# Performance work log

Hardware: AMD Instinct MI355X
Metric: run time of the kernel (lower is better)

Reference implementation:

```python
import jax, jax.numpy as jnp
import numpy as np

B, S, D = 4, 2048, 1024


def setup_inputs() -> dict:
    key = jax.random.key(0)
    ks = jax.random.split(key, 8)
    x = jax.random.normal(ks[0], (B, S, D), dtype=jnp.float32)
    # additive causal mask: 0 on/below diagonal, -1e9 above
    causal = jnp.tril(jnp.ones((S, S), dtype=bool))
    mask = jnp.where(causal, 0.0, -1e9).astype(jnp.float32)[None, :, :]  # [1,S,S]
    scale = 1.0 / np.sqrt(D)
    Wq = jax.random.normal(ks[1], (D, D), dtype=jnp.float32) * scale
    bq = jnp.zeros((D,), dtype=jnp.float32)
    Wk = jax.random.normal(ks[2], (D, D), dtype=jnp.float32) * scale
    bk = jnp.zeros((D,), dtype=jnp.float32)
    Wv = jax.random.normal(ks[3], (D, D), dtype=jnp.float32) * scale
    bv = jnp.zeros((D,), dtype=jnp.float32)
    return {"x": x, "mask": mask, "Wq": Wq, "bq": bq, "Wk": Wk, "bk": bk, "Wv": Wv, "bv": bv}


def reference(x, mask, Wq, bq, Wk, bk, Wv, bv):
    # Q/K/V projections (torch Linear: y = x @ W^T + b)
    q = jnp.einsum('bsd,ed->bse', x, Wq) + bq
    k = jnp.einsum('bsd,ed->bse', x, Wk) + bk
    v = jnp.einsum('bsd,ed->bse', x, Wv) + bv
    d = x.shape[-1]
    scores = jnp.einsum('bqd,bkd->bqk', q, k) / jnp.sqrt(jnp.float32(d))
    scores = scores + mask
    attn = jax.nn.softmax(scores, axis=-1)
    return jnp.einsum('bqk,bkd->bqd', attn, v)
```

## Files before the change

kernel.cpp:

```cpp
#include <hip/hip_runtime.h>
#include <hip/hip_bf16.h>


typedef __attribute__((ext_vector_type(8))) short short8;
typedef __attribute__((ext_vector_type(4))) float f32x4;
typedef __attribute__((ext_vector_type(4))) unsigned short ushort4v;

static __device__ __forceinline__ unsigned short f2b(float f) {
  union { __hip_bfloat16 h; unsigned short u; } cv;
  cv.h = __float2bfloat16(f);
  return cv.u;
}

#define GLOAD_LDS16(gsrc, ldst)                                              \
  __builtin_amdgcn_global_load_lds(                                          \
      (const __attribute__((address_space(1))) void*)(gsrc),                 \
      (__attribute__((address_space(3))) void*)(ldst), 16, 0, 0)

__global__ __launch_bounds__(256) void cvt4(const float* __restrict__ in,
                                            unsigned short* __restrict__ out, int n4) {
  int i = blockIdx.x * blockDim.x + threadIdx.x;
  if (i >= n4) return;
  float4 v = reinterpret_cast<const float4*>(in)[i];
  ushort4v o;
  o.x = f2b(v.x); o.y = f2b(v.y); o.z = f2b(v.z); o.w = f2b(v.w);
  reinterpret_cast<ushort4v*>(out)[i] = o;
}

__global__ __launch_bounds__(256) void prep_w(
    const float* __restrict__ Wq, const float* __restrict__ Wk, const float* __restrict__ Wv,
    const float* __restrict__ bq, const float* __restrict__ bk, const float* __restrict__ bv,
    unsigned short* __restrict__ Wb, float* __restrict__ biasb) {
  int id = blockIdx.x;
  if (id < 3072) {
    int sel = id >> 10;
    const float* src = sel == 0 ? Wq : sel == 1 ? Wk : Wv;
    int i = (id & 1023) * 256 + threadIdx.x;
    float4 v = reinterpret_cast<const float4*>(src)[i];
    ushort4v o;
    o.x = f2b(v.x); o.y = f2b(v.y); o.z = f2b(v.z); o.w = f2b(v.w);
    reinterpret_cast<ushort4v*>(Wb + (long)sel * 1048576)[i] = o;
  } else {
    int i = (id - 3072) * 256 + threadIdx.x;
    if (i < 3072) {
      int sel = i >> 10;
      const float* src = sel == 0 ? bq : sel == 1 ? bk : bv;
      biasb[i] = src[i & 1023];
    }
  }
}

template <typename EPI>
static __device__ __forceinline__ void gemm128_body(
    const unsigned short* __restrict__ Ab, const unsigned short* __restrict__ Bb,
    int lda, int ldb, int nkt, unsigned short* sA, unsigned short* sB, EPI epi) {
  int tid = threadIdx.x;
  int lane = tid & 63;
  int w = tid >> 6;
  int wr = w >> 1, wc = w & 1;

  f32x4 acc[4][4];
#pragma unroll
  for (int m = 0; m < 4; ++m)
#pragma unroll
    for (int n = 0; n < 4; ++n) acc[m][n] = (f32x4){0.f, 0.f, 0.f, 0.f};

  for (int kt = 0; kt < nkt; ++kt) {
    __syncthreads();
#pragma unroll
    for (int c = 0; c < 8; ++c) {
      int chunk = w * 8 + c;
      int half = chunk & 15;
      int L = half * 1024 + lane * 16;
      int row = L >> 7;
      int gs = ((L >> 4) & 7) ^ (row & 7);
      if (chunk < 16) {
        GLOAD_LDS16(Ab + (long)row * lda + kt * 64 + gs * 8, sA + half * 512);
      } else {
        GLOAD_LDS16(Bb + (long)row * ldb + kt * 64 + gs * 8, sB + half * 512);
      }
    }
    __syncthreads();

#pragma unroll
    for (int kk = 0; kk < 2; ++kk) {
      short8 af[4], bfr[4];
#pragma unroll
      for (int m = 0; m < 4; ++m) {
        int row = wr * 64 + m * 16 + (lane & 15);
        int g = kk * 4 + (lane >> 4);
        af[m] = *(const short8*)((const char*)sA + row * 128 + ((g ^ (row & 7)) << 4));
      }
#pragma unroll
      for (int n = 0; n < 4; ++n) {
        int row = wc * 64 + n * 16 + (lane & 15);
        int g = kk * 4 + (lane >> 4);
        bfr[n] = *(const short8*)((const char*)sB + row * 128 + ((g ^ (row & 7)) << 4));
      }
#pragma unroll
      for (int m = 0; m < 4; ++m)
#pragma unroll
        for (int n = 0; n < 4; ++n)
          acc[m][n] = __builtin_amdgcn_mfma_f32_16x16x32_bf16(af[m], bfr[n], acc[m][n], 0, 0, 0);
    }
  }
  int rloc = wr * 64 + (lane >> 4) * 4;
  int cloc = wc * 64 + (lane & 15);
  epi(acc, rloc, cloc);
}

__global__ __launch_bounds__(256) void proj_gemm(
    const unsigned short* __restrict__ A, const unsigned short* __restrict__ B,
    unsigned short* __restrict__ C, const float* __restrict__ bias) {
  __shared__ unsigned short sA[128 * 64];
  __shared__ unsigned short sB[128 * 64];
  int bx = blockIdx.x, by = blockIdx.y;
  const unsigned short* Ab = A + (long)by * 128 * 1024;
  const unsigned short* Bb = B + (long)bx * 128 * 1024;
  gemm128_body(Ab, Bb, 1024, 1024, 16, sA, sB,
               [&](f32x4 acc[4][4], int rloc, int cloc) {
                 int r0 = by * 128 + rloc;
                 int c0 = bx * 128 + cloc;
#pragma unroll
                 for (int m = 0; m < 4; ++m)
#pragma unroll
                   for (int n = 0; n < 4; ++n) {
                     int gc = c0 + n * 16;
                     float bv = bias[gc];
#pragma unroll
                     for (int r = 0; r < 4; ++r)
                       C[(long)(r0 + m * 16 + r) * 3072 + gc] = f2b(acc[m][n][r] + bv);
                   }
               });
}

__global__ __launch_bounds__(256) void scores_gemm(
    const unsigned short* __restrict__ QKV, float* __restrict__ S) {
  __shared__ unsigned short sA[128 * 64];
  __shared__ unsigned short sB[128 * 64];
  int t = blockIdx.x;
  int by = (int)((sqrtf(8.f * t + 1.f) - 1.f) * 0.5f);
  while ((by + 1) * (by + 2) / 2 <= t) ++by;
  while (by * (by + 1) / 2 > t) --by;
  int bx = t - by * (by + 1) / 2;
  long bz = blockIdx.z;
  const unsigned short* Q = QKV + bz * (2048L * 3072);
  const unsigned short* Ab = Q + (long)by * 128 * 3072;
  const unsigned short* Bb = Q + 1024 + (long)bx * 128 * 3072;
  float* Sb = S + bz * (2048L * 2048);
  gemm128_body(Ab, Bb, 3072, 3072, 16, sA, sB,
               [&](f32x4 acc[4][4], int rloc, int cloc) {
                 int r0 = by * 128 + rloc;
                 int c0 = bx * 128 + cloc;
#pragma unroll
                 for (int m = 0; m < 4; ++m)
#pragma unroll
                   for (int n = 0; n < 4; ++n)
#pragma unroll
                     for (int r = 0; r < 4; ++r)
                       Sb[(long)(r0 + m * 16 + r) * 2048 + c0 + n * 16] =
                           acc[m][n][r] * 0.03125f;
               });
}

__global__ __launch_bounds__(256) void transpose64(const unsigned short* __restrict__ V,
                                                   unsigned short* __restrict__ Vt) {
  __shared__ unsigned short t[64][72];
  int s0 = blockIdx.x * 64, d0 = blockIdx.y * 64;
  long bz = blockIdx.z;
  const unsigned short* src = V + bz * (2048L * 3072);
  unsigned short* dst = Vt + bz * (1024L * 2048);
  int tid = threadIdx.x;
#pragma unroll
  for (int pp = 0; pp < 2; ++pp) {
    int r = pp * 32 + (tid >> 3);
    int c = (tid & 7) * 8;
    short8 v = *(const short8*)(src + (long)(s0 + r) * 3072 + d0 + c);
    *(short8*)&t[r][c] = v;
  }
  __syncthreads();
#pragma unroll
  for (int pp = 0; pp < 2; ++pp) {
    int d = pp * 32 + (tid >> 3);
    int sc = (tid & 7) * 8;
    short8 v;
#pragma unroll
    for (int k = 0; k < 8; ++k) v[k] = (short)t[sc + k][d];
    *(short8*)(dst + (long)(d0 + d) * 2048 + s0 + sc) = v;
  }
}

__global__ __launch_bounds__(256) void softmax_causal(float* __restrict__ S) {
  int row = blockIdx.x;
  long b = row >> 11;
  int i = row & 2047;
  float* s = S + (b * 2048 + i) * 2048;
  unsigned short* p = (unsigned short*)s;
  int n = i + 1;
  int jEnd = ((i >> 7) + 1) << 7;
  int tid = threadIdx.x;
  __shared__ float red[4];

  float vals[8];
  float m = -3.0e38f;
#pragma unroll
  for (int k = 0; k < 8; ++k) {
    int j = tid + k * 256;
    vals[k] = (j < n) ? s[j] : -3.0e38f;
    m = fmaxf(m, vals[k]);
  }
#pragma unroll
  for (int off = 32; off > 0; off >>= 1) m = fmaxf(m, __shfl_xor(m, off));
  if ((tid & 63) == 0) red[tid >> 6] = m;
  __syncthreads();
  m = fmaxf(fmaxf(red[0], red[1]), fmaxf(red[2], red[3]));
  __syncthreads();

  float sum = 0.f;
#pragma unroll
  for (int k = 0; k < 8; ++k) {
    int j = tid + k * 256;
    float e = (j < n) ? __expf(vals[k] - m) : 0.f;
    vals[k] = e;
    sum += e;
  }
#pragma unroll
  for (int off = 32; off > 0; off >>= 1) sum += __shfl_xor(sum, off);
  if ((tid & 63) == 0) red[tid >> 6] = sum;
  __syncthreads();
  sum = red[0] + red[1] + red[2] + red[3];
  float inv = 1.0f / sum;

#pragma unroll
  for (int k = 0; k < 8; ++k) {
    int j = tid + k * 256;
    if (j < jEnd) p[j] = f2b(vals[k] * inv);
  }
}

__global__ __launch_bounds__(512) void pv_gemm(
    const unsigned short* __restrict__ P, const unsigned short* __restrict__ Vt,
    float* __restrict__ out) {
  __shared__ unsigned short sA[128 * 64];
  __shared__ unsigned short sB[128 * 64];
  int tid = threadIdx.x;
  int lane = tid & 63;
  int w = tid >> 6;
  int wr = w >> 2, wc = w & 3;
  int bx = blockIdx.x, byp = blockIdx.y, bz = blockIdx.z;
  const unsigned short* Pb = P + bz * (2048L * 4096);
  const unsigned short* Bb = Vt + bz * (1024L * 2048) + (long)bx * 128 * 2048;
  float* Ob = out + bz * (2048L * 1024);

#pragma unroll
  for (int half = 0; half < 2; ++half) {
    int strip = half == 0 ? (15 - byp) : byp;
    int nkt = (strip + 1) * 2;
    const unsigned short* Ab = Pb + (long)strip * 128 * 4096;

    f32x4 acc[4][2];
#pragma unroll
    for (int m = 0; m < 4; ++m)
#pragma unroll
      for (int n = 0; n < 2; ++n) acc[m][n] = (f32x4){0.f, 0.f, 0.f, 0.f};

    for (int kt = 0; kt < nkt; ++kt) {
      __syncthreads();
#pragma unroll
      for (int c = 0; c < 4; ++c) {
        int chunk = w * 4 + c;
        int hh = chunk & 15;
        int L = hh * 1024 + lane * 16;
        int row = L >> 7;
        int gs = ((L >> 4) & 7) ^ (row & 7);
        if (chunk < 16) {
          GLOAD_LDS16(Ab + (long)row * 4096 + kt * 64 + gs * 8, sA + hh * 512);
        } else {
          GLOAD_LDS16(Bb + (long)row * 2048 + kt * 64 + gs * 8, sB + hh * 512);
        }
      }
      __syncthreads();

#pragma unroll
      for (int kk = 0; kk < 2; ++kk) {
        short8 af[4], bf2[2];
#pragma unroll
        for (int m = 0; m < 4; ++m) {
          int row = wr * 64 + m * 16 + (lane & 15);
          int g = kk * 4 + (lane >> 4);
          af[m] = *(const short8*)((const char*)sA + row * 128 + ((g ^ (row & 7)) << 4));
        }
#pragma unroll
        for (int n = 0; n < 2; ++n) {
          int row = wc * 32 + n * 16 + (lane & 15);
          int g = kk * 4 + (lane >> 4);
          bf2[n] = *(const short8*)((const char*)sB + row * 128 + ((g ^ (row & 7)) << 4));
        }
#pragma unroll
        for (int m = 0; m < 4; ++m)
#pragma unroll
          for (int n = 0; n < 2; ++n)
            acc[m][n] = __builtin_amdgcn_mfma_f32_16x16x32_bf16(af[m], bf2[n], acc[m][n], 0, 0, 0);
      }
    }

    int r0 = strip * 128 + wr * 64 + (lane >> 4) * 4;
    int c0 = bx * 128 + wc * 32 + (lane & 15);
#pragma unroll
    for (int m = 0; m < 4; ++m)
#pragma unroll
      for (int n = 0; n < 2; ++n)
#pragma unroll
        for (int r = 0; r < 4; ++r)
          Ob[(long)(r0 + m * 16 + r) * 1024 + c0 + n * 16] = acc[m][n][r];
  }
}

extern "C" void kernel_launch(void* const* d_in, const int* in_sizes, int n_in,
                              void* d_out, int out_size, void* d_ws, size_t ws_size,
                              hipStream_t stream) {
  const float* x = (const float*)d_in[0];
  const float* Wq = (const float*)d_in[2];
  const float* bq = (const float*)d_in[3];
  const float* Wk = (const float*)d_in[4];
  const float* bk = (const float*)d_in[5];
  const float* Wv = (const float*)d_in[6];
  const float* bv = (const float*)d_in[7];
  float* out = (float*)d_out;

  char* ws = (char*)d_ws;
  const long MB = 1 << 20;
  unsigned short* xb = (unsigned short*)(ws);
  unsigned short* Wb = (unsigned short*)(ws + 16 * MB);
  float* biasb = (float*)(ws + 22 * MB);
  unsigned short* QKV = (unsigned short*)(ws + 23 * MB);
  unsigned short* Vt = (unsigned short*)(ws + 71 * MB);
  float* Sbuf = (float*)(ws + 87 * MB);

  cvt4<<<8192, 256, 0, stream>>>(x, xb, 2097152);
  prep_w<<<3084, 256, 0, stream>>>(Wq, Wk, Wv, bq, bk, bv, Wb, biasb);

  proj_gemm<<<dim3(24, 64), 256, 0, stream>>>(xb, Wb, QKV, biasb);

  transpose64<<<dim3(32, 16, 4), 256, 0, stream>>>(QKV + 2048, Vt);

  scores_gemm<<<dim3(136, 1, 4), 256, 0, stream>>>(QKV, Sbuf);

  softmax_causal<<<8192, 256, 0, stream>>>(Sbuf);

  pv_gemm<<<dim3(8, 8, 4), 512, 0, stream>>>((unsigned short*)Sbuf, Vt, out);
}
```

Before: 285.3 us.

## Double-buffer LDS tiles in scores and PV GEMMs to overlap loads with MFMA

The scores and PV GEMM kernels now use two LDS buffers, issuing the global-to-LDS loads for the next K tile before computing on the current one. A vmcnt wait and a barrier separate the stages, replacing two __syncthreads per tile with one barrier per half-step. The projection GEMM is inlined with runtime strides but is otherwise unchanged. Doubling LDS usage can reduce occupancy, and the PV loop assumes an even tile count.

Result: faster. 271.7 us (-4.8%).

```diff
diff --git a/kernel.cpp b/kernel.cpp
--- a/kernel.cpp
+++ b/kernel.cpp
@@ -16,6 +16,8 @@
   __builtin_amdgcn_global_load_lds(                                          \
       (const __attribute__((address_space(1))) void*)(gsrc),                 \
       (__attribute__((address_space(3))) void*)(ldst), 16, 0, 0)
+
+#define WAIT_VM0() asm volatile("s_waitcnt vmcnt(0)" ::: "memory")
 
 __global__ __launch_bounds__(256) void cvt4(const float* __restrict__ in,
                                             unsigned short* __restrict__ out, int n4) {
@@ -50,22 +52,30 @@
   }
 }
 
-template <typename EPI>
-static __device__ __forceinline__ void gemm128_body(
-    const unsigned short* __restrict__ Ab, const unsigned short* __restrict__ Bb,
-    int lda, int ldb, int nkt, unsigned short* sA, unsigned short* sB, EPI epi) {
+__global__ __launch_bounds__(256) void proj_gemm(
+    const unsigned short* __restrict__ A, const unsigned short* __restrict__ B,
+    unsigned short* __restrict__ Cout, const float* __restrict__ bias,
+    int lda, int ldb, int ldc, int ktiles) {
+  int bx = blockIdx.x, by = blockIdx.y;
+
+  __shared__ unsigned short sA[128 * 64];
+  __shared__ unsigned short sB[128 * 64];
+
   int tid = threadIdx.x;
   int lane = tid & 63;
   int w = tid >> 6;
   int wr = w >> 1, wc = w & 1;
 
+  const unsigned short* Ab = A + (long)by * 128 * lda;
+  const unsigned short* Bb = B + (long)bx * 128 * ldb;
+
   f32x4 acc[4][4];
 #pragma unroll
   for (int m = 0; m < 4; ++m)
 #pragma unroll
     for (int n = 0; n < 4; ++n) acc[m][n] = (f32x4){0.f, 0.f, 0.f, 0.f};
 
-  for (int kt = 0; kt < nkt; ++kt) {
+  for (int kt = 0; kt < ktiles; ++kt) {
     __syncthreads();
 #pragma unroll
     for (int c = 0; c < 8; ++c) {
@@ -104,40 +114,25 @@
           acc[m][n] = __builtin_amdgcn_mfma_f32_16x16x32_bf16(af[m], bfr[n], acc[m][n], 0, 0, 0);
     }
   }
-  int rloc = wr * 64 + (lane >> 4) * 4;
-  int cloc = wc * 64 + (lane & 15);
-  epi(acc, rloc, cloc);
-}
-
-__global__ __launch_bounds__(256) void proj_gemm(
-    const unsigned short* __restrict__ A, const unsigned short* __restrict__ B,
-    unsigned short* __restrict__ C, const float* __restrict__ bias) {
-  __shared__ unsigned short sA[128 * 64];
-  __shared__ unsigned short sB[128 * 64];
-  int bx = blockIdx.x, by = blockIdx.y;
-  const unsigned short* Ab = A + (long)by * 128 * 1024;
-  const unsigned short* Bb = B + (long)bx * 128 * 1024;
-  gemm128_body(Ab, Bb, 1024, 1024, 16, sA, sB,
-               [&](f32x4 acc[4][4], int rloc, int cloc) {
-                 int r0 = by * 128 + rloc;
-                 int c0 = bx * 128 + cloc;
-#pragma unroll
-                 for (int m = 0; m < 4; ++m)
-#pragma unroll
-                   for (int n = 0; n < 4; ++n) {
-                     int gc = c0 + n * 16;
-                     float bv = bias[gc];
-#pragma unroll
-                     for (int r = 0; r < 4; ++r)
-                       C[(long)(r0 + m * 16 + r) * 3072 + gc] = f2b(acc[m][n][r] + bv);
-                   }
-               });
+
+  int r0 = by * 128 + wr * 64 + (lane >> 4) * 4;
+  int c0 = bx * 128 + wc * 64 + (lane & 15);
+#pragma unroll
+  for (int m = 0; m < 4; ++m)
+#pragma unroll
+    for (int n = 0; n < 4; ++n) {
+      int gc = c0 + n * 16;
+      float bv = bias[gc];
+#pragma unroll
+      for (int r = 0; r < 4; ++r)
+        Cout[(long)(r0 + m * 16 + r) * ldc + gc] = f2b(acc[m][n][r] + bv);
+    }
 }
 
 __global__ __launch_bounds__(256) void scores_gemm(
     const unsigned short* __restrict__ QKV, float* __restrict__ S) {
-  __shared__ unsigned short sA[128 * 64];
-  __shared__ unsigned short sB[128 * 64];
+  __shared__ unsigned short sA[2][128 * 64];
+  __shared__ unsigned short sB[2][128 * 64];
   int t = blockIdx.x;
   int by = (int)((sqrtf(8.f * t + 1.f) - 1.f) * 0.5f);
   while ((by + 1) * (by + 2) / 2 <= t) ++by;
@@ -147,20 +142,86 @@
   const unsigned short* Q = QKV + bz * (2048L * 3072);
   const unsigned short* Ab = Q + (long)by * 128 * 3072;
   const unsigned short* Bb = Q + 1024 + (long)bx * 128 * 3072;
+
+  int tid = threadIdx.x;
+  int lane = tid & 63;
+  int w = tid >> 6;
+  int wr = w >> 1, wc = w & 1;
+
+  f32x4 acc[4][4];
+#pragma unroll
+  for (int m = 0; m < 4; ++m)
+#pragma unroll
+    for (int n = 0; n < 4; ++n) acc[m][n] = (f32x4){0.f, 0.f, 0.f, 0.f};
+
+#define SC_STAGE(BUF, KT)                                                        \
+  do {                                                                           \
+    _Pragma("unroll") for (int c = 0; c < 8; ++c) {                              \
+      int chunk = w * 8 + c;                                                     \
+      int half = chunk & 15;                                                     \
+      int L = half * 1024 + lane * 16;                                           \
+      int row = L >> 7;                                                          \
+      int gs = ((L >> 4) & 7) ^ (row & 7);                                       \
+      if (chunk < 16) {                                                          \
+        GLOAD_LDS16(Ab + (long)row * 3072 + (KT) * 64 + gs * 8,                  \
+                    &sA[BUF][half * 512]);                                       \
+      } else {                                                                   \
+        GLOAD_LDS16(Bb + (long)row * 3072 + (KT) * 64 + gs * 8,                  \
+                    &sB[BUF][half * 512]);                                       \
+      }                                                                          \
+    }                                                                            \
+  } while (0)
+
+#define SC_COMPUTE(BUF)                                                          \
+  do {                                                                           \
+    _Pragma("unroll") for (int kk = 0; kk < 2; ++kk) {                           \
+      short8 af[4], bfr[4];                                                      \
+      _Pragma("unroll") for (int m = 0; m < 4; ++m) {                            \
+        int row = wr * 64 + m * 16 + (lane & 15);                                \
+        int g = kk * 4 + (lane >> 4);                                            \
+        af[m] = *(const short8*)((const char*)sA[BUF] + row * 128 +              \
+                                 ((g ^ (row & 7)) << 4));                        \
+      }                                                                          \
+      _Pragma("unroll") for (int n = 0; n < 4; ++n) {                            \
+        int row = wc * 64 + n * 16 + (lane & 15);                                \
+        int g = kk * 4 + (lane >> 4);                                            \
+        bfr[n] = *(const short8*)((const char*)sB[BUF] + row * 128 +             \
+                                  ((g ^ (row & 7)) << 4));                       \
+      }                                                                          \
+      _Pragma("unroll") for (int m = 0; m < 4; ++m)                              \
+          _Pragma("unroll") for (int n = 0; n < 4; ++n) acc[m][n] =              \
+          __builtin_amdgcn_mfma_f32_16x16x32_bf16(af[m], bfr[n], acc[m][n],      \
+                                                  0, 0, 0);                      \
+    }                                                                            \
+  } while (0)
+
+  SC_STAGE(0, 0);
+  WAIT_VM0();
+  __builtin_amdgcn_s_barrier();
+#pragma unroll 1
+  for (int kt = 0; kt < 16; kt += 2) {
+    if (kt + 1 < 16) SC_STAGE(1, kt + 1);
+    SC_COMPUTE(0);
+    WAIT_VM0();
+    __builtin_amdgcn_s_barrier();
+    if (kt + 2 < 16) SC_STAGE(0, kt + 2);
+    SC_COMPUTE(1);
+    WAIT_VM0();
+    __builtin_amdgcn_s_barrier();
+  }
+
   float* Sb = S + bz * (2048L * 2048);
-  gemm128_body(Ab, Bb, 3072, 3072, 16, sA, sB,
-               [&](f32x4 acc[4][4], int rloc, int cloc) {
-                 int r0 = by * 128 + rloc;
-                 int c0 = bx * 128 + cloc;
-#pragma unroll
-                 for (int m = 0; m < 4; ++m)
-#pragma unroll
-                   for (int n = 0; n < 4; ++n)
-#pragma unroll
-                     for (int r = 0; r < 4; ++r)
-                       Sb[(long)(r0 + m * 16 + r) * 2048 + c0 + n * 16] =
-                           acc[m][n][r] * 0.03125f;
-               });
+  int r0 = by * 128 + wr * 64 + (lane >> 4) * 4;
+  int c0 = bx * 128 + wc * 64 + (lane & 15);
+#pragma unroll
+  for (int m = 0; m < 4; ++m)
+#pragma unroll
+    for (int n = 0; n < 4; ++n)
+#pragma unroll
+      for (int r = 0; r < 4; ++r)
+        Sb[(long)(r0 + m * 16 + r) * 2048 + c0 + n * 16] = acc[m][n][r] * 0.03125f;
+#undef SC_STAGE
+#undef SC_COMPUTE
 }
 
 __global__ __launch_bounds__(256) void transpose64(const unsigned short* __restrict__ V,
@@ -241,8 +302,8 @@
 __global__ __launch_bounds__(512) void pv_gemm(
     const unsigned short* __restrict__ P, const unsigned short* __restrict__ Vt,
     float* __restrict__ out) {
-  __shared__ unsigned short sA[128 * 64];
-  __shared__ unsigned short sB[128 * 64];
+  __shared__ unsigned short sA[2][128 * 64];
+  __shared__ unsigned short sB[2][128 * 64];
   int tid = threadIdx.x;
   int lane = tid & 63;
   int w = tid >> 6;
@@ -252,7 +313,48 @@
   const unsigned short* Bb = Vt + bz * (1024L * 2048) + (long)bx * 128 * 2048;
   float* Ob = out + bz * (2048L * 1024);
 
-#pragma unroll
+#define PV_STAGE(BUF, KT)                                                        \
+  do {                                                                           \
+    _Pragma("unroll") for (int c = 0; c < 4; ++c) {                              \
+      int chunk = w * 4 + c;                                                     \
+      int hh = chunk & 15;                                                       \
+      int L = hh * 1024 + lane * 16;                                             \
+      int row = L >> 7;                                                          \
+      int gs = ((L >> 4) & 7) ^ (row & 7);                                       \
+      if (chunk < 16) {                                                          \
+        GLOAD_LDS16(Ab + (long)row * 4096 + (KT) * 64 + gs * 8,                  \
+                    &sA[BUF][hh * 512]);                                         \
+      } else {                                                                   \
+        GLOAD_LDS16(Bb + (long)row * 2048 + (KT) * 64 + gs * 8,                  \
+                    &sB[BUF][hh * 512]);                                         \
+      }                                                                          \
+    }                                                                            \
+  } while (0)
+
+#define PV_COMPUTE(BUF)                                                          \
+  do {                                                                           \
+    _Pragma("unroll") for (int kk = 0; kk < 2; ++kk) {                           \
+      short8 af[4], bf2[2];                                                      \
+      _Pragma("unroll") for (int m = 0; m < 4; ++m) {                            \
+        int row = wr * 64 + m * 16 + (lane & 15);                                \
+        int g = kk * 4 + (lane >> 4);                                            \
+        af[m] = *(const short8*)((const char*)sA[BUF] + row * 128 +              \
+                                 ((g ^ (row & 7)) << 4));                        \
+      }                                                                          \
+      _Pragma("unroll") for (int n = 0; n < 2; ++n) {                            \
+        int row = wc * 32 + n * 16 + (lane & 15);                                \
+        int g = kk * 4 + (lane >> 4);                                            \
+        bf2[n] = *(const short8*)((const char*)sB[BUF] + row * 128 +             \
+                                  ((g ^ (row & 7)) << 4));                       \
+      }                                                                          \
+      _Pragma("unroll") for (int m = 0; m < 4; ++m)                              \
+          _Pragma("unroll") for (int n = 0; n < 2; ++n) acc[m][n] =              \
+          __builtin_amdgcn_mfma_f32_16x16x32_bf16(af[m], bf2[n], acc[m][n],      \
+                                                  0, 0, 0);                      \
+    }                                                                            \
+  } while (0)
+
+#pragma unroll 1
   for (int half = 0; half < 2; ++half) {
     int strip = half == 0 ? (15 - byp) : byp;
     int nkt = (strip + 1) * 2;
@@ -264,44 +366,19 @@
 #pragma unroll
       for (int n = 0; n < 2; ++n) acc[m][n] = (f32x4){0.f, 0.f, 0.f, 0.f};
 
-    for (int kt = 0; kt < nkt; ++kt) {
-      __syncthreads();
-#pragma unroll
-      for (int c = 0; c < 4; ++c) {
-        int chunk = w * 4 + c;
-        int hh = chunk & 15;
-        int L = hh * 1024 + lane * 16;
-        int row = L >> 7;
-        int gs = ((L >> 4) & 7) ^ (row & 7);
-        if (chunk < 16) {
-          GLOAD_LDS16(Ab + (long)row * 4096 + kt * 64 + gs * 8, sA + hh * 512);
-        } else {
-          GLOAD_LDS16(Bb + (long)row * 2048 + kt * 64 + gs * 8, sB + hh * 512);
-        }
-      }
-      __syncthreads();
-
-#pragma unroll
-      for (int kk = 0; kk < 2; ++kk) {
-        short8 af[4], bf2[2];
-#pragma unroll
-        for (int m = 0; m < 4; ++m) {
-          int row = wr * 64 + m * 16 + (lane & 15);
-          int g = kk * 4 + (lane >> 4);
-          af[m] = *(const short8*)((const char*)sA + row * 128 + ((g ^ (row & 7)) << 4));
-        }
-#pragma unroll
-        for (int n = 0; n < 2; ++n) {
-          int row = wc * 32 + n * 16 + (lane & 15);
-          int g = kk * 4 + (lane >> 4);
-          bf2[n] = *(const short8*)((const char*)sB + row * 128 + ((g ^ (row & 7)) << 4));
-        }
-#pragma unroll
-        for (int m = 0; m < 4; ++m)
-#pragma unroll
-          for (int n = 0; n < 2; ++n)
-            acc[m][n] = __builtin_amdgcn_mfma_f32_16x16x32_bf16(af[m], bf2[n], acc[m][n], 0, 0, 0);
-      }
+    PV_STAGE(0, 0);
+    WAIT_VM0();
+    __builtin_amdgcn_s_barrier();
+#pragma unroll 1
+    for (int kt = 0; kt < nkt; kt += 2) {
+      PV_STAGE(1, kt + 1);
+      PV_COMPUTE(0);
+      WAIT_VM0();
+      __builtin_amdgcn_s_barrier();
+      if (kt + 2 < nkt) PV_STAGE(0, kt + 2);
+      PV_COMPUTE(1);
+      WAIT_VM0();
+      __builtin_amdgcn_s_barrier();
     }
 
     int r0 = strip * 128 + wr * 64 + (lane >> 4) * 4;
@@ -314,6 +391,8 @@
         for (int r = 0; r < 4; ++r)
           Ob[(long)(r0 + m * 16 + r) * 1024 + c0 + n * 16] = acc[m][n][r];
   }
+#undef PV_STAGE
+#undef PV_COMPUTE
 }
 
 extern "C" void kernel_launch(void* const* d_in, const int* in_sizes, int n_in,
@@ -340,7 +419,7 @@
   cvt4<<<8192, 256, 0, stream>>>(x, xb, 2097152);
   prep_w<<<3084, 256, 0, stream>>>(Wq, Wk, Wv, bq, bk, bv, Wb, biasb);
 
-  proj_gemm<<<dim3(24, 64), 256, 0, stream>>>(xb, Wb, QKV, biasb);
+  proj_gemm<<<dim3(24, 64), 256, 0, stream>>>(xb, Wb, QKV, biasb, 1024, 1024, 3072, 16);
 
   transpose64<<<dim3(32, 16, 4), 256, 0, stream>>>(QKV + 2048, Vt);
 
```
